# Optimization experiments

Measured on AMD Instinct MI355X. Metric: run time of the kernel, lower is better.

Reference implementation:

```python
import jax, jax.numpy as jnp
import numpy as np

N, C, B = 131072, 256, 2
Z, Y, X = 32, 240, 240  # spconv coord order: batch, z, y, x
EPS = 1e-5


def _build_sparse():
    """Generate unique sparse voxel coords and per-axis 3-tap submanifold
    neighbor tables (rulebook). Sentinel index N marks a missing neighbor."""
    rng = np.random.default_rng(0)
    per = N // B
    coords = []
    for b in range(B):
        lin = rng.choice(Z * Y * X, per, replace=False)
        z, r = np.divmod(lin, Y * X)
        y, x = np.divmod(r, X)
        coords.append(np.stack([np.full(per, b), z, y, x], 1))
    coords = np.concatenate(coords, 0).astype(np.int64)
    keys = ((coords[:, 0] * Z + coords[:, 1]) * Y + coords[:, 2]) * X + coords[:, 3]
    order = np.argsort(keys)
    coords, keys = coords[order], keys[order]

    def nbr_axis(axis, bound):
        out = np.full((N, 3), N, dtype=np.int64)
        for k, off in enumerate((-1, 0, 1)):
            c = coords.copy()
            c[:, axis] += off
            valid = (c[:, axis] >= 0) & (c[:, axis] < bound)
            qk = ((c[:, 0] * Z + c[:, 1]) * Y + c[:, 2]) * X + c[:, 3]
            pos = np.clip(np.searchsorted(keys, qk), 0, N - 1)
            hit = valid & (keys[pos] == qk)
            out[:, k] = np.where(hit, pos, N)
        return out

    return nbr_axis(1, Z), nbr_axis(2, Y), nbr_axis(3, X)


def setup_inputs() -> dict:
    nbr1, nbr2, nbr3 = _build_sparse()
    key = jax.random.key(0)
    ks = jax.random.split(key, 4)
    scale = 0.02  # keep pre-sigmoid activations in a sane range
    return {
        "features": jax.random.normal(ks[0], (N, C), jnp.float32),
        "W1": jax.random.normal(ks[1], (3, C, C), jnp.float32) * scale,
        "W2": jax.random.normal(ks[2], (3, C, C), jnp.float32) * scale,
        "W3": jax.random.normal(ks[3], (3, C, C), jnp.float32) * scale,
        "g1": jnp.ones((C,), jnp.float32), "b1": jnp.zeros((C,), jnp.float32),
        "g2": jnp.ones((C,), jnp.float32), "b2": jnp.zeros((C,), jnp.float32),
        "g3": jnp.ones((C,), jnp.float32), "b3": jnp.zeros((C,), jnp.float32),
        "nbr1": jnp.asarray(nbr1), "nbr2": jnp.asarray(nbr2), "nbr3": jnp.asarray(nbr3),
    }


def _subm_conv(fp, nbr, W):
    # fp: [N+1, C] (last row zero pad), nbr: [N, 3], W: [3, Cin, Cout]
    return fp[nbr[:, 0]] @ W[0] + fp[nbr[:, 1]] @ W[1] + fp[nbr[:, 2]] @ W[2]


def _bn(h, g, b):
    mu = h.mean(0)
    var = h.var(0)  # biased, matches torch BN normalization in train mode
    return g * (h - mu) * jax.lax.rsqrt(var + EPS) + b


def reference(features, W1, W2, W3, g1, b1, g2, b2, g3, b3, nbr1, nbr2, nbr3):
    pad = jnp.zeros((1, features.shape[1]), features.dtype)
    fp = jnp.concatenate([features, pad], 0)  # [N+1, C]
    s1 = jax.nn.sigmoid(_bn(_subm_conv(fp, nbr1, W1), g1, b1))
    s2 = jax.nn.sigmoid(_bn(_subm_conv(fp, nbr2, W2), g2, b2))
    s3 = jax.nn.sigmoid(_bn(_subm_conv(fp, nbr3, W3), g3, b3))
    return (s1 + s2 + s3) * features
```

## Files before the change

### kernel.cpp

```cpp
#include <hip/hip_runtime.h>
#include <hip/hip_bf16.h>


#define NP 131072
#define CC 256
#define TILEE (128 * 32)

typedef __attribute__((ext_vector_type(4))) float f32x4;
typedef __attribute__((ext_vector_type(8))) short bf16x8;

__device__ __forceinline__ unsigned short f2bf(float f) {
    unsigned int u = __float_as_uint(f);
    u += 0x7FFFu + ((u >> 16) & 1u);
    return (unsigned short)(u >> 16);
}
__device__ __forceinline__ float bf2f(unsigned short s) {
    return __uint_as_float(((unsigned int)s) << 16);
}

__device__ __forceinline__ void gload_lds16(const void* g, void* l) {
    __builtin_amdgcn_global_load_lds(
        (const __attribute__((address_space(1))) unsigned int*)g,
        (__attribute__((address_space(3))) unsigned int*)l, 16, 0, 0);
}

__global__ void zero_stats_k(float* stats) {
    int i = blockIdx.x * 256 + threadIdx.x;
    if (i < 3 * 2 * CC) stats[i] = 0.f;
}

__global__ void cast_features_k(const float* __restrict__ f, unsigned short* __restrict__ fb) {
    size_t e = ((size_t)blockIdx.x * 256 + threadIdx.x) * 8;
    const size_t tot = (size_t)(NP + 1) * CC;
    if (e >= tot) return;
    unsigned short tmp[8];
    if (e >= (size_t)NP * CC) {
        #pragma unroll
        for (int j = 0; j < 8; ++j) tmp[j] = 0;
    } else {
        float4 v0 = *(const float4*)(f + e);
        float4 v1 = *(const float4*)(f + e + 4);
        tmp[0] = f2bf(v0.x); tmp[1] = f2bf(v0.y); tmp[2] = f2bf(v0.z); tmp[3] = f2bf(v0.w);
        tmp[4] = f2bf(v1.x); tmp[5] = f2bf(v1.y); tmp[6] = f2bf(v1.z); tmp[7] = f2bf(v1.w);
    }
    *(bf16x8*)(fb + e) = *(bf16x8*)tmp;
}

__global__ void cast_weights_k(const float* __restrict__ W1, const float* __restrict__ W2,
                               const float* __restrict__ W3, unsigned short* __restrict__ wbT) {
    int bid  = blockIdx.x;
    int m    = bid >> 8;
    int cout = bid & 255;
    int cin  = threadIdx.x;
    const float* W = (m < 3) ? W1 : (m < 6) ? W2 : W3;
    int tap = m - (m / 3) * 3;
    float v = W[((size_t)tap * CC + cin) * CC + cout];
    wbT[((size_t)m * CC + cout) * CC + cin] = f2bf(v);
}

#define MFMA16(a, b, c) __builtin_amdgcn_mfma_f32_16x16x32_bf16((a), (b), (c), 0, 0, 0)

__global__ __launch_bounds__(256, 3)
void gemm_conv_fused_k(const unsigned short* __restrict__ fb,
                       const unsigned short* __restrict__ wbT,
                       const int* __restrict__ nbr1, const int* __restrict__ nbr2,
                       const int* __restrict__ nbr3,
                       unsigned short* __restrict__ hbase,
                       float* __restrict__ statsBase) {
    __shared__ unsigned short As[2][TILEE];
    __shared__ unsigned short Bs[2][TILEE];
    __shared__ float colsum[128];
    __shared__ float colsq[128];

    const int axis = blockIdx.y;
    const int* nbr = (axis == 0) ? nbr1 : (axis == 1) ? nbr2 : nbr3;
    const unsigned short* wA = wbT + (size_t)axis * 3 * CC * CC;
    unsigned short* h = hbase + (size_t)axis * NP * CC;
    float* stats = statsBase + axis * 2 * CC;

    const int tid  = threadIdx.x;
    const int lane = tid & 63;
    const int wave = tid >> 6;
    const int bx   = blockIdx.x;
    const int swzb = (bx & 7) * 256 + (bx >> 3);
    const int rowBase = (swzb >> 1) * 128;
    const int colBase = (swzb & 1) * 128;

    if (tid < 128) { colsum[tid] = 0.f; colsq[tid] = 0.f; }

    int srcOff[2], gA0[2], gA1[2], gA2[2], bRow[2];
    #pragma unroll
    for (int u = 0; u < 2; ++u) {
        int idx = u * 256 + tid;
        int r = idx >> 2, p = idx & 3;
        srcOff[u] = (p ^ ((r >> 1) & 3)) * 8;
        int gi = rowBase + r;
        gA0[u] = nbr[(size_t)gi * 3 + 0];
        gA1[u] = nbr[(size_t)gi * 3 + 1];
        gA2[u] = nbr[(size_t)gi * 3 + 2];
        bRow[u] = colBase + r;
    }

#define STAGE_A(u, Abuf, tapsel, kkE) do {                                      \
        int gr_ = ((tapsel) == 0) ? gA0[u] : ((tapsel) == 1) ? gA1[u] : gA2[u]; \
        gload_lds16(fb + (size_t)gr_ * CC + (kkE) + srcOff[u],                  \
                    (Abuf) + ((u) * 256 + tid) * 8);                            \
    } while (0)
#define STAGE_B(u, Bbuf, wTt, kkE)                                              \
        gload_lds16((wTt) + (size_t)bRow[u] * CC + (kkE) + srcOff[u],           \
                    (Bbuf) + ((u) * 256 + tid) * 8)

    const int wr = (wave >> 1) & 1;
    const int wc = wave & 1;
    const int fr = lane & 15;
    const int kq = lane >> 4;
    const int chunkOff = (kq ^ ((fr >> 1) & 3)) * 8;
    const int rA = wr * 64 + fr;
    const int rB = wc * 64 + fr;

    f32x4 acc[4][4] = {};

    STAGE_A(0, As[0], 0, 0); STAGE_A(1, As[0], 0, 0);
    STAGE_B(0, Bs[0], wA, 0); STAGE_B(1, Bs[0], wA, 0);
    __syncthreads();

    for (int t = 0; t < 24; ++t) {
        const unsigned short* Ac = As[t & 1];
        const unsigned short* Bc = Bs[t & 1];
        unsigned short* An = As[(t + 1) & 1];
        unsigned short* Bn = Bs[(t + 1) & 1];
        const int t1 = t + 1;
        const int tap1 = t1 >> 3;
        const int kk1 = (t1 & 7) * 32;

        if (t < 23) {
            const unsigned short* wT1 = wA + (size_t)tap1 * CC * CC;
            STAGE_A(0, An, tap1, kk1); STAGE_A(1, An, tap1, kk1);
            STAGE_B(0, Bn, wT1, kk1);  STAGE_B(1, Bn, wT1, kk1);
        }

        bf16x8 aF[4], bF[4];
        #pragma unroll
        for (int m = 0; m < 4; ++m)
            aF[m] = *(const bf16x8*)(Ac + (rA + m * 16) * 32 + chunkOff);
        #pragma unroll
        for (int n = 0; n < 4; ++n)
            bF[n] = *(const bf16x8*)(Bc + (rB + n * 16) * 32 + chunkOff);
        #pragma unroll
        for (int m = 0; m < 4; ++m)
            #pragma unroll
            for (int n = 0; n < 4; ++n)
                acc[m][n] = MFMA16(aF[m], bF[n], acc[m][n]);

        __syncthreads();
    }

    const int orow = (lane >> 4) * 4;
    float psum[4], psq[4];
    #pragma unroll
    for (int n = 0; n < 4; ++n) { psum[n] = 0.f; psq[n] = 0.f; }
    #pragma unroll
    for (int m = 0; m < 4; ++m) {
        #pragma unroll
        for (int n = 0; n < 4; ++n) {
            int col = colBase + wc * 64 + n * 16 + fr;
            int row = rowBase + wr * 64 + m * 16 + orow;
            #pragma unroll
            for (int j = 0; j < 4; ++j) {
                unsigned short hb = f2bf(acc[m][n][j]);
                float v = bf2f(hb);
                h[(size_t)(row + j) * CC + col] = hb;
                psum[n] += v;
                psq[n]  += v * v;
            }
        }
    }
    #pragma unroll
    for (int n = 0; n < 4; ++n) {
        psum[n] += __shfl_xor(psum[n], 16);
        psum[n] += __shfl_xor(psum[n], 32);
        psq[n]  += __shfl_xor(psq[n], 16);
        psq[n]  += __shfl_xor(psq[n], 32);
    }
    if ((lane >> 4) == 0) {
        #pragma unroll
        for (int n = 0; n < 4; ++n) {
            int cl = wc * 64 + n * 16 + fr;
            atomicAdd(&colsum[cl], psum[n]);
            atomicAdd(&colsq[cl],  psq[n]);
        }
    }
    __syncthreads();
    if (tid < 128) {
        int c = colBase + tid;
        atomicAdd(&stats[c],      colsum[tid]);
        atomicAdd(&stats[CC + c], colsq[tid]);
    }
#undef STAGE_A
#undef STAGE_B
}

__global__ void finalize3_k(const float* __restrict__ stats,
                            const float* __restrict__ g1, const float* __restrict__ b1,
                            const float* __restrict__ g2, const float* __restrict__ b2,
                            const float* __restrict__ g3, const float* __restrict__ b3,
                            float* __restrict__ ss) {
    int a = blockIdx.x;
    int c = threadIdx.x;
    const float* g = (a == 0) ? g1 : (a == 1) ? g2 : g3;
    const float* b = (a == 0) ? b1 : (a == 1) ? b2 : b3;
    const float* st = stats + a * 2 * CC;
    float* s = ss + a * 2 * CC;
    float mu  = st[c] * (1.f / NP);
    float var = st[CC + c] * (1.f / NP) - mu * mu;
    float sc  = g[c] * rsqrtf(var + 1e-5f);
    s[c]      = sc;
    s[CC + c] = b[c] - mu * sc;
}

__global__ void apply3_k(const unsigned short* __restrict__ h1,
                         const unsigned short* __restrict__ h2,
                         const unsigned short* __restrict__ h3,
                         const float* __restrict__ ss,
                         const unsigned short* __restrict__ fb, float* __restrict__ out) {
    size_t e = ((size_t)blockIdx.x * 256 + threadIdx.x) * 8;
    int c0 = (int)(e & (CC - 1));
    bf16x8 v1 = __builtin_nontemporal_load((const bf16x8*)(h1 + e));
    bf16x8 v2 = __builtin_nontemporal_load((const bf16x8*)(h2 + e));
    bf16x8 v3 = __builtin_nontemporal_load((const bf16x8*)(h3 + e));
    bf16x8 fv = *(const bf16x8*)(fb + e);
    float s[8];
    #pragma unroll
    for (int j = 0; j < 8; ++j) {
        float z1 = ss[c0 + j]          * bf2f((unsigned short)v1[j]) + ss[CC + c0 + j];
        float z2 = ss[2 * CC + c0 + j] * bf2f((unsigned short)v2[j]) + ss[3 * CC + c0 + j];
        float z3 = ss[4 * CC + c0 + j] * bf2f((unsigned short)v3[j]) + ss[5 * CC + c0 + j];
        float sg = 1.f / (1.f + __expf(-z1)) + 1.f / (1.f + __expf(-z2)) + 1.f / (1.f + __expf(-z3));
        s[j] = sg * bf2f((unsigned short)fv[j]);
    }
    f32x4* o = (f32x4*)(out + e);
    f32x4 o0 = {s[0], s[1], s[2], s[3]};
    f32x4 o1 = {s[4], s[5], s[6], s[7]};
    __builtin_nontemporal_store(o0, o);
    __builtin_nontemporal_store(o1, o + 1);
}

extern "C" void kernel_launch(void* const* d_in, const int* in_sizes, int n_in,
                              void* d_out, int out_size, void* d_ws, size_t ws_size,
                              hipStream_t stream) {
    const float* feat = (const float*)d_in[0];
    const float* W1   = (const float*)d_in[1];
    const float* W2   = (const float*)d_in[2];
    const float* W3   = (const float*)d_in[3];
    const float* g1   = (const float*)d_in[4];
    const float* b1   = (const float*)d_in[5];
    const float* g2   = (const float*)d_in[6];
    const float* b2   = (const float*)d_in[7];
    const float* g3   = (const float*)d_in[8];
    const float* b3   = (const float*)d_in[9];
    const int* nbr1   = (const int*)d_in[10];
    const int* nbr2   = (const int*)d_in[11];
    const int* nbr3   = (const int*)d_in[12];
    float* out = (float*)d_out;

    char* w = (char*)d_ws;
    unsigned short* fb   = (unsigned short*)w;  w += (size_t)(NP + 1) * CC * 2;
    unsigned short* wbT  = (unsigned short*)w;  w += (size_t)9 * CC * CC * 2;
    float* stats         = (float*)w;           w += (size_t)3 * 2 * CC * 4;
    float* ss            = (float*)w;           w += (size_t)3 * 2 * CC * 4;
    unsigned short* hbuf = (unsigned short*)w;

    zero_stats_k<<<6, 256, 0, stream>>>(stats);
    {
        size_t tot = (size_t)(NP + 1) * CC / 8;
        int blocks = (int)((tot + 255) / 256);
        cast_features_k<<<blocks, 256, 0, stream>>>(feat, fb);
    }
    cast_weights_k<<<2304, 256, 0, stream>>>(W1, W2, W3, wbT);

    gemm_conv_fused_k<<<dim3(2048, 3), 256, 0, stream>>>(fb, wbT, nbr1, nbr2, nbr3,
                                                         hbuf, stats);
    finalize3_k<<<3, 256, 0, stream>>>(stats, g1, b1, g2, b2, g3, b3, ss);
    apply3_k<<<16384, 256, 0, stream>>>(hbuf,
                                        hbuf + (size_t)NP * CC,
                                        hbuf + (size_t)2 * NP * CC,
                                        ss, fb, out);
}
```

Measured before the change: 276.5 us.

## Load weight fragments directly from global memory, dropping LDS staging for B

Removes the shared-memory double buffer for the weight tile and has each lane read its bf16 weight fragments straight from global (L2-cached) memory inside the k-loop. It also raises the occupancy hint from 3 to 4 blocks per CU, which the halved LDS footprint allows. Separately, the apply kernel switches its intermediate loads from nontemporal to ordinary loads. The cost is that global weight loads now sit on the critical path just before the MFMAs, with no prefetch, so memory latency may stall the math unless the extra occupancy hides it.

Result: slower. 458.4 us (+65.8%).

```diff
diff --git a/kernel.cpp b/kernel.cpp
--- a/kernel.cpp
+++ b/kernel.cpp
@@ -60,7 +60,7 @@
 
 #define MFMA16(a, b, c) __builtin_amdgcn_mfma_f32_16x16x32_bf16((a), (b), (c), 0, 0, 0)
 
-__global__ __launch_bounds__(256, 3)
+__global__ __launch_bounds__(256, 4)
 void gemm_conv_fused_k(const unsigned short* __restrict__ fb,
                        const unsigned short* __restrict__ wbT,
                        const int* __restrict__ nbr1, const int* __restrict__ nbr2,
@@ -68,7 +68,6 @@
                        unsigned short* __restrict__ hbase,
                        float* __restrict__ statsBase) {
     __shared__ unsigned short As[2][TILEE];
-    __shared__ unsigned short Bs[2][TILEE];
     __shared__ float colsum[128];
     __shared__ float colsq[128];
 
@@ -88,7 +87,7 @@
 
     if (tid < 128) { colsum[tid] = 0.f; colsq[tid] = 0.f; }
 
-    int srcOff[2], gA0[2], gA1[2], gA2[2], bRow[2];
+    int srcOff[2], gA0[2], gA1[2], gA2[2];
     #pragma unroll
     for (int u = 0; u < 2; ++u) {
         int idx = u * 256 + tid;
@@ -98,7 +97,6 @@
         gA0[u] = nbr[(size_t)gi * 3 + 0];
         gA1[u] = nbr[(size_t)gi * 3 + 1];
         gA2[u] = nbr[(size_t)gi * 3 + 2];
-        bRow[u] = colBase + r;
     }
 
 #define STAGE_A(u, Abuf, tapsel, kkE) do {                                      \
@@ -106,9 +104,6 @@
         gload_lds16(fb + (size_t)gr_ * CC + (kkE) + srcOff[u],                  \
                     (Abuf) + ((u) * 256 + tid) * 8);                            \
     } while (0)
-#define STAGE_B(u, Bbuf, wTt, kkE)                                              \
-        gload_lds16((wTt) + (size_t)bRow[u] * CC + (kkE) + srcOff[u],           \
-                    (Bbuf) + ((u) * 256 + tid) * 8)
 
     const int wr = (wave >> 1) & 1;
     const int wc = wave & 1;
@@ -116,36 +111,37 @@
     const int kq = lane >> 4;
     const int chunkOff = (kq ^ ((fr >> 1) & 3)) * 8;
     const int rA = wr * 64 + fr;
-    const int rB = wc * 64 + fr;
+    const unsigned short* bBase = wA + (size_t)(colBase + wc * 64 + fr) * CC + kq * 8;
 
     f32x4 acc[4][4] = {};
 
     STAGE_A(0, As[0], 0, 0); STAGE_A(1, As[0], 0, 0);
-    STAGE_B(0, Bs[0], wA, 0); STAGE_B(1, Bs[0], wA, 0);
     __syncthreads();
 
     for (int t = 0; t < 24; ++t) {
         const unsigned short* Ac = As[t & 1];
-        const unsigned short* Bc = Bs[t & 1];
-        unsigned short* An = As[(t + 1) & 1];
-        unsigned short* Bn = Bs[(t + 1) & 1];
-        const int t1 = t + 1;
-        const int tap1 = t1 >> 3;
-        const int kk1 = (t1 & 7) * 32;
+        const int tap = t >> 3;
+        const int kk  = (t & 7) * 32;
 
         if (t < 23) {
-            const unsigned short* wT1 = wA + (size_t)tap1 * CC * CC;
-            STAGE_A(0, An, tap1, kk1); STAGE_A(1, An, tap1, kk1);
-            STAGE_B(0, Bn, wT1, kk1);  STAGE_B(1, Bn, wT1, kk1);
+            const int t1 = t + 1;
+            const int tap1 = t1 >> 3;
+            const int kk1 = (t1 & 7) * 32;
+            STAGE_A(0, As[t1 & 1], tap1, kk1);
+            STAGE_A(1, As[t1 & 1], tap1, kk1);
         }
 
-        bf16x8 aF[4], bF[4];
+        const unsigned short* bT = bBase + (size_t)tap * CC * CC + kk;
+        bf16x8 bF[4];
+        #pragma unroll
+        for (int n = 0; n < 4; ++n)
+            bF[n] = *(const bf16x8*)(bT + (size_t)(n * 16) * CC);
+
+        bf16x8 aF[4];
         #pragma unroll
         for (int m = 0; m < 4; ++m)
             aF[m] = *(const bf16x8*)(Ac + (rA + m * 16) * 32 + chunkOff);
-        #pragma unroll
-        for (int n = 0; n < 4; ++n)
-            bF[n] = *(const bf16x8*)(Bc + (rB + n * 16) * 32 + chunkOff);
+
         #pragma unroll
         for (int m = 0; m < 4; ++m)
             #pragma unroll
@@ -197,7 +193,6 @@
         atomicAdd(&stats[CC + c], colsq[tid]);
     }
 #undef STAGE_A
-#undef STAGE_B
 }
 
 __global__ void finalize3_k(const float* __restrict__ stats,
@@ -225,9 +220,9 @@
                          const unsigned short* __restrict__ fb, float* __restrict__ out) {
     size_t e = ((size_t)blockIdx.x * 256 + threadIdx.x) * 8;
     int c0 = (int)(e & (CC - 1));
-    bf16x8 v1 = __builtin_nontemporal_load((const bf16x8*)(h1 + e));
-    bf16x8 v2 = __builtin_nontemporal_load((const bf16x8*)(h2 + e));
-    bf16x8 v3 = __builtin_nontemporal_load((const bf16x8*)(h3 + e));
+    bf16x8 v1 = *(const bf16x8*)(h1 + e);
+    bf16x8 v2 = *(const bf16x8*)(h2 + e);
+    bf16x8 v3 = *(const bf16x8*)(h3 + e);
     bf16x8 fv = *(const bf16x8*)(fb + e);
     float s[8];
     #pragma unroll
```

## Load gathered A fragments directly into registers instead of staging through LDS

Applied to the files above, without the earlier changes.

The fused gather-GEMM no longer stages the neighbor-gathered feature rows into shared memory. Each lane now loads its MFMA A-fragments straight from global memory into registers, double-buffered one k-step ahead, while only the weight tile still goes through LDS. This halves LDS usage and removes the LDS write/read round trip for A, which may raise occupancy. The cost is narrow 16-byte per-lane global loads with more register pressure and possible exposed latency. The apply kernel also drops its nontemporal loads in favour of plain loads.

Result: slower. 348.4 us (+26.0%).

```diff
diff --git a/kernel.cpp b/kernel.cpp
--- a/kernel.cpp
+++ b/kernel.cpp
@@ -4,7 +4,7 @@
 
 #define NP 131072
 #define CC 256
-#define TILEE (128 * 32)
+#define BTILE (128 * 32)
 
 typedef __attribute__((ext_vector_type(4))) float f32x4;
 typedef __attribute__((ext_vector_type(8))) short bf16x8;
@@ -67,8 +67,7 @@
                        const int* __restrict__ nbr3,
                        unsigned short* __restrict__ hbase,
                        float* __restrict__ statsBase) {
-    __shared__ unsigned short As[2][TILEE];
-    __shared__ unsigned short Bs[2][TILEE];
+    __shared__ unsigned short Bs[2][BTILE];
     __shared__ float colsum[128];
     __shared__ float colsq[128];
 
@@ -88,26 +87,17 @@
 
     if (tid < 128) { colsum[tid] = 0.f; colsq[tid] = 0.f; }
 
-    int srcOff[2], gA0[2], gA1[2], gA2[2], bRow[2];
+    int srcOffB[2], bRow[2];
     #pragma unroll
     for (int u = 0; u < 2; ++u) {
         int idx = u * 256 + tid;
         int r = idx >> 2, p = idx & 3;
-        srcOff[u] = (p ^ ((r >> 1) & 3)) * 8;
-        int gi = rowBase + r;
-        gA0[u] = nbr[(size_t)gi * 3 + 0];
-        gA1[u] = nbr[(size_t)gi * 3 + 1];
-        gA2[u] = nbr[(size_t)gi * 3 + 2];
+        srcOffB[u] = (p ^ ((r >> 1) & 3)) * 8;
         bRow[u] = colBase + r;
     }
 
-#define STAGE_A(u, Abuf, tapsel, kkE) do {                                      \
-        int gr_ = ((tapsel) == 0) ? gA0[u] : ((tapsel) == 1) ? gA1[u] : gA2[u]; \
-        gload_lds16(fb + (size_t)gr_ * CC + (kkE) + srcOff[u],                  \
-                    (Abuf) + ((u) * 256 + tid) * 8);                            \
-    } while (0)
 #define STAGE_B(u, Bbuf, wTt, kkE)                                              \
-        gload_lds16((wTt) + (size_t)bRow[u] * CC + (kkE) + srcOff[u],           \
+        gload_lds16((wTt) + (size_t)bRow[u] * CC + (kkE) + srcOffB[u],          \
                     (Bbuf) + ((u) * 256 + tid) * 8)
 
     const int wr = (wave >> 1) & 1;
@@ -115,44 +105,60 @@
     const int fr = lane & 15;
     const int kq = lane >> 4;
     const int chunkOff = (kq ^ ((fr >> 1) & 3)) * 8;
-    const int rA = wr * 64 + fr;
     const int rB = wc * 64 + fr;
 
+    int gidx[4][3];
+    #pragma unroll
+    for (int m = 0; m < 4; ++m) {
+        int gr = rowBase + wr * 64 + m * 16 + fr;
+        #pragma unroll
+        for (int tp = 0; tp < 3; ++tp)
+            gidx[m][tp] = nbr[(size_t)gr * 3 + tp];
+    }
+    const int kqOff = kq * 8;
+
     f32x4 acc[4][4] = {};
-
-    STAGE_A(0, As[0], 0, 0); STAGE_A(1, As[0], 0, 0);
+    bf16x8 aP[2][4];
+
     STAGE_B(0, Bs[0], wA, 0); STAGE_B(1, Bs[0], wA, 0);
+    #pragma unroll
+    for (int m = 0; m < 4; ++m)
+        aP[0][m] = *(const bf16x8*)(fb + (size_t)gidx[m][0] * CC + kqOff);
     __syncthreads();
 
-    for (int t = 0; t < 24; ++t) {
-        const unsigned short* Ac = As[t & 1];
-        const unsigned short* Bc = Bs[t & 1];
-        unsigned short* An = As[(t + 1) & 1];
-        unsigned short* Bn = Bs[(t + 1) & 1];
-        const int t1 = t + 1;
-        const int tap1 = t1 >> 3;
-        const int kk1 = (t1 & 7) * 32;
-
-        if (t < 23) {
-            const unsigned short* wT1 = wA + (size_t)tap1 * CC * CC;
-            STAGE_A(0, An, tap1, kk1); STAGE_A(1, An, tap1, kk1);
-            STAGE_B(0, Bn, wT1, kk1);  STAGE_B(1, Bn, wT1, kk1);
-        }
-
-        bf16x8 aF[4], bF[4];
-        #pragma unroll
-        for (int m = 0; m < 4; ++m)
-            aF[m] = *(const bf16x8*)(Ac + (rA + m * 16) * 32 + chunkOff);
-        #pragma unroll
-        for (int n = 0; n < 4; ++n)
-            bF[n] = *(const bf16x8*)(Bc + (rB + n * 16) * 32 + chunkOff);
-        #pragma unroll
-        for (int m = 0; m < 4; ++m)
+    #pragma unroll
+    for (int tap = 0; tap < 3; ++tap) {
+        #pragma unroll
+        for (int s = 0; s < 8; ++s) {
+            const int t   = tap * 8 + s;
+            const int cur = t & 1;
+            const int nxt = cur ^ 1;
+
+            if (t < 23) {
+                const int t1   = t + 1;
+                const int tap1 = t1 >> 3;
+                const int kk1  = (t1 & 7) * 32;
+                #pragma unroll
+                for (int m = 0; m < 4; ++m)
+                    aP[nxt][m] = *(const bf16x8*)(fb + (size_t)gidx[m][tap1] * CC + kk1 + kqOff);
+                const unsigned short* wT1 = wA + (size_t)tap1 * CC * CC;
+                STAGE_B(0, Bs[nxt], wT1, kk1);
+                STAGE_B(1, Bs[nxt], wT1, kk1);
+            }
+
+            bf16x8 bF[4];
             #pragma unroll
             for (int n = 0; n < 4; ++n)
-                acc[m][n] = MFMA16(aF[m], bF[n], acc[m][n]);
-
-        __syncthreads();
+                bF[n] = *(const bf16x8*)(Bs[cur] + (rB + n * 16) * 32 + chunkOff);
+
+            #pragma unroll
+            for (int m = 0; m < 4; ++m)
+                #pragma unroll
+                for (int n = 0; n < 4; ++n)
+                    acc[m][n] = MFMA16(aP[cur][m], bF[n], acc[m][n]);
+
+            __syncthreads();
+        }
     }
 
     const int orow = (lane >> 4) * 4;
@@ -196,7 +202,6 @@
         atomicAdd(&stats[c],      colsum[tid]);
         atomicAdd(&stats[CC + c], colsq[tid]);
     }
-#undef STAGE_A
 #undef STAGE_B
 }
 
@@ -225,9 +230,9 @@
                          const unsigned short* __restrict__ fb, float* __restrict__ out) {
     size_t e = ((size_t)blockIdx.x * 256 + threadIdx.x) * 8;
     int c0 = (int)(e & (CC - 1));
-    bf16x8 v1 = __builtin_nontemporal_load((const bf16x8*)(h1 + e));
-    bf16x8 v2 = __builtin_nontemporal_load((const bf16x8*)(h2 + e));
-    bf16x8 v3 = __builtin_nontemporal_load((const bf16x8*)(h3 + e));
+    bf16x8 v1 = *(const bf16x8*)(h1 + e);
+    bf16x8 v2 = *(const bf16x8*)(h2 + e);
+    bf16x8 v3 = *(const bf16x8*)(h3 + e);
     bf16x8 fv = *(const bf16x8*)(fb + e);
     float s[8];
     #pragma unroll
```
